# Kernel optimization log

Hardware: AMD Instinct MI355X
Metric: run time of the kernel (lower is better)

## Reference

```python
import jax, jax.numpy as jnp
import numpy as np
import math

KV_STRIDE = 2
Q_STRIDE = 1
WAVE_LEN = 1000.0
POS_MAG = 1.0


def _pos_embed(h, w, h_kv, w_kv, q_stride, kv_stride, feat_dim):
    # Sinusoidal relative-position embeddings, matching get_position_embedding.
    h_idx = jnp.arange(h, dtype=jnp.float32) * q_stride
    w_idx = jnp.arange(w, dtype=jnp.float32) * q_stride
    h_kv_idx = jnp.arange(h_kv, dtype=jnp.float32) * kv_stride
    w_kv_idx = jnp.arange(w_kv, dtype=jnp.float32) * kv_stride
    h_diff = (h_idx[:, None] - h_kv_idx[None, :]) * POS_MAG  # (h, h_kv)
    w_diff = (w_idx[:, None] - w_kv_idx[None, :]) * POS_MAG  # (w, w_kv)
    feat_range = jnp.arange(feat_dim // 4, dtype=jnp.float32)
    dim_mat = WAVE_LEN ** (4.0 / feat_dim * feat_range)  # (feat_dim//4,)
    wd = w_diff[:, :, None] / dim_mat  # (w, w_kv, F)
    hd = h_diff[:, :, None] / dim_mat  # (h, h_kv, F)
    emb_x = jnp.concatenate([jnp.sin(wd), jnp.cos(wd)], axis=2)  # (w, w_kv, feat_dim//2)
    emb_y = jnp.concatenate([jnp.sin(hd), jnp.cos(hd)], axis=2)  # (h, h_kv, feat_dim//2)
    return emb_x, emb_y


def setup_inputs() -> dict:
    key = jax.random.key(0)
    ks = jax.random.split(key, 11)
    C = 288
    s = 1.0 / math.sqrt(C)
    return {
        'x_input': jax.random.normal(ks[0], (2, C, 64, 64), jnp.float32),
        'Wq': jax.random.normal(ks[1], (C, C), jnp.float32) * s,
        'Wk': jax.random.normal(ks[2], (C, C), jnp.float32) * s,
        'Wv': jax.random.normal(ks[3], (C, C), jnp.float32) * s,
        'Wx': jax.random.normal(ks[4], (C, C // 2), jnp.float32) * s,
        'Wy': jax.random.normal(ks[5], (C, C // 2), jnp.float32) * s,
        'Wproj': jax.random.normal(ks[6], (C, C), jnp.float32) * s,
        'bproj': jax.random.normal(ks[7], (C,), jnp.float32) * 0.02,
        'Wc': jax.random.normal(ks[8], (9, C), jnp.float32) * s,
        'bc': jax.random.normal(ks[9], (9,), jnp.float32) * 0.02,
        'gamma': jax.random.normal(ks[10], (1,), jnp.float32),
    }


def reference(x_input, Wq, Wk, Wv, Wx, Wy, Wproj, bproj, Wc, bc, gamma):
    M = Wc.shape[0]                       # num_mixtures
    n, C, h, w = x_input.shape
    d = Wq.shape[0] // M                  # qk_embed_dim (== v_dim)
    x_q = x_input                         # q_stride == 1
    x_kv = x_input[:, :, ::KV_STRIDE, ::KV_STRIDE]  # AvgPool2d(k=1, stride=2)
    h_kv, w_kv = x_kv.shape[2], x_kv.shape[3]

    # 1x1 convs as channel GEMMs
    q = jnp.einsum('nchw,oc->nohw', x_q, Wq).reshape(n, M, d, h * w)
    q = q.transpose(0, 1, 3, 2)                                    # (n,M,hw,d)
    k = jnp.einsum('nchw,oc->nohw', x_kv, Wk).reshape(n, M, d, h_kv * w_kv)

    emb_x, emb_y = _pos_embed(h, w, h_kv, w_kv, Q_STRIDE, KV_STRIDE, C)
    inv_sqrt2 = 1.0 / math.sqrt(2.0)
    pf_x = (emb_x @ Wx.T).reshape(w, w_kv, M, d).transpose(2, 0, 1, 3) * inv_sqrt2  # (M,w,w_kv,d)
    pf_y = (emb_y @ Wy.T).reshape(h, h_kv, M, d).transpose(2, 0, 1, 3) * inv_sqrt2  # (M,h,h_kv,d)

    energy = jnp.matmul(q, k).reshape(n, M, h, w, h_kv, w_kv)
    q5 = q.reshape(n, M, h, w, d)
    e_x = jnp.einsum('nmhwd,mwvd->nmhwv', q5, pf_x)  # (n,M,h,w,w_kv)
    e_y = jnp.einsum('nmhwd,mhud->nmhwu', q5, pf_y)  # (n,M,h,w,h_kv)
    energy = energy + e_x[:, :, :, :, None, :] + e_y[:, :, :, :, :, None]
    energy = energy.reshape(n, M, h * w, h_kv * w_kv)
    attn = jax.nn.softmax(energy, axis=3)

    # Learned per-mixture gating from mean query context
    context = q.transpose(0, 1, 3, 2).reshape(n, M * d, h * w).mean(axis=2)  # (n, M*d)
    mix_w = jax.nn.softmax(context @ Wc.T + bc, axis=1)                      # (n, M)
    attn = jnp.sum(attn * mix_w[:, :, None, None], axis=1)                   # (n,hw,hw_kv)

    v = jnp.einsum('nchw,oc->nohw', x_kv, Wv).reshape(n, M * d, h_kv * w_kv)
    v = v.transpose(0, 2, 1)                                                 # (n,hw_kv,M*d)
    out = jnp.matmul(attn, v).transpose(0, 2, 1).reshape(n, M * d, h, w)
    out = jnp.einsum('nchw,oc->nohw', out, Wproj) + bproj[None, :, None, None]
    return gamma[0] * out + x_input
```

## Files before the change

kernel.cpp:

```cpp
#include <hip/hip_runtime.h>
#include <math.h>

#define NB     2
#define CDIM   288
#define HW     4096
#define PKV    1024
#define MHEAD  9
#define DHEAD  32

typedef __attribute__((ext_vector_type(8))) short bf16x8;
typedef __attribute__((ext_vector_type(4))) float f32x4;
typedef __attribute__((ext_vector_type(2))) unsigned int u32x2;
typedef __attribute__((ext_vector_type(4))) unsigned int u32x4;

#if __has_builtin(__builtin_amdgcn_exp2f)
#define EXP2(x) __builtin_amdgcn_exp2f(x)
#else
#define EXP2(x) exp2f(x)
#endif

__device__ inline unsigned short f2bf(float x) {
    unsigned int u = __float_as_uint(x);
    u = (u + 0x7fffu + ((u >> 16) & 1u)) >> 16;
    return (unsigned short)u;
}

__device__ inline void nt_store_u2(unsigned short* p, u32x2 v) {
    __builtin_nontemporal_store(v, (u32x2*)p);
}
__device__ inline void nt_store_u4(unsigned short* p, u32x4 v) {
    __builtin_nontemporal_store(v, (u32x4*)p);
}
__device__ inline void nt_store_bf8(unsigned short* p, bf16x8 v) {
    __builtin_nontemporal_store(v, (bf16x8*)p);
}


__global__ __launch_bounds__(256) void prep(const float* __restrict__ X,
        const float* __restrict__ Wq, const float* __restrict__ Wk,
        const float* __restrict__ Wv, const float* __restrict__ Wproj,
        unsigned short* __restrict__ XF, unsigned short* __restrict__ WFq,
        unsigned short* __restrict__ WFk, unsigned short* __restrict__ WFv,
        unsigned short* __restrict__ WFp, float* __restrict__ MX) {
    __shared__ float t32[32][133];
    __shared__ float red[4];
    int b = blockIdx.x;
    int tid = threadIdx.x;
    if (b < 576) {
        int bx = b % 32, by = (b / 32) % 9, n = b / 288;
        int j0 = bx * 128, c0 = by * 32;
        int c = tid >> 3, f = tid & 7;
        const float* src = &X[((size_t)n * CDIM + c0 + c) * HW + j0];
#pragma unroll
        for (int l = 0; l < 4; ++l) {
            float4 v = *(const float4*)&src[(f + l * 8) * 4];
            *(float4*)&t32[c][(f + l * 8) * 4] = v;
        }
        __syncthreads();
        int cc = c0 >> 5;
#pragma unroll
        for (int l = 0; l < 4; ++l) {
            int g = l * 256 + tid;
            int s = g >> 7;
            int w = g & 127;
            int lane = w >> 1, e0 = (w & 1) * 4;
            int jl = s * 16 + (lane & 15);
            int cb = (lane >> 4) * 8 + e0;
            unsigned int w0 = f2bf(t32[cb + 0][jl]) | ((unsigned int)f2bf(t32[cb + 1][jl]) << 16);
            unsigned int w1 = f2bf(t32[cb + 2][jl]) | ((unsigned int)f2bf(t32[cb + 3][jl]) << 16);
            int jt = (j0 >> 4) + s;
            unsigned short* O = XF + (size_t)n * HW * CDIM + ((size_t)jt * 9 + cc) * 512 + lane * 8 + e0;
            u32x2 pk = { w0, w1 };
            nt_store_u2(O, pk);
        }
    } else if (b < 738) {
        int t = b - 576;
        int sub = tid >> 6, lane = tid & 63;
        int ot = t / 9, cc = t % 9;
        const float* W = (sub == 0) ? Wq : (sub == 1) ? Wk : (sub == 2) ? Wv : Wproj;
        unsigned short* O = ((sub == 0) ? WFq : (sub == 1) ? WFk : (sub == 2) ? WFv : WFp)
                            + (size_t)t * 512;
        int o  = ot * 16 + (lane & 15);
        int c0 = cc * 32 + (lane >> 4) * 8;
        const float* src = W + (size_t)o * CDIM + c0;
        float4 f0 = *(const float4*)src, f1 = *(const float4*)(src + 4);
        unsigned int v0 = f2bf(f0.x) | ((unsigned int)f2bf(f0.y) << 16);
        unsigned int v1 = f2bf(f0.z) | ((unsigned int)f2bf(f0.w) << 16);
        unsigned int v2 = f2bf(f1.x) | ((unsigned int)f2bf(f1.y) << 16);
        unsigned int v3 = f2bf(f1.z) | ((unsigned int)f2bf(f1.w) << 16);
        u32x4 pk = { v0, v1, v2, v3 };
        nt_store_u4(O + lane * 8, pk);
    } else {
        int bid = b - 738;
        const float* xr = X + (size_t)bid * HW;
        float s = 0.f;
        for (int j = tid; j < HW; j += 256) s += xr[j];
        for (int off = 32; off > 0; off >>= 1) s += __shfl_xor(s, off, 64);
        if ((tid & 63) == 0) red[tid >> 6] = s;
        __syncthreads();
        if (tid == 0) MX[bid] = (red[0] + red[1] + red[2] + red[3]) * (1.f / 4096.f);
    }
}

__global__ __launch_bounds__(256) void mid(
        const float* __restrict__ Wx, const float* __restrict__ Wy,
        unsigned short* __restrict__ FXb, unsigned short* __restrict__ FYb,
        const float* __restrict__ Wq, const float* __restrict__ MX,
        const float* __restrict__ Wc, const float* __restrict__ bc,
        float* __restrict__ MIXW,
        const unsigned short* __restrict__ WFq, const unsigned short* __restrict__ WFk,
        const unsigned short* __restrict__ WFv, const unsigned short* __restrict__ XF,
        unsigned short* __restrict__ Qf, unsigned short* __restrict__ KF,
        unsigned short* __restrict__ VF) {
    __shared__ float emb[144];
    __shared__ float ctx_s[NB * CDIM];
    __shared__ float lg[18];
    __shared__ __attribute__((aligned(16))) unsigned short tr[4][32][40];
    int b = blockIdx.x;
    int tid = threadIdx.x;

    if (b < 252) {
        int axis = b / 126;
        int dif  = b % 126;
        float diff = (float)(dif - 62);
        if (tid < 72) {
            float dm = expf(6.9077552789821368f * ((float)tid * (1.f / 72.f)));
            float t  = diff / dm;
            emb[tid]      = sinf(t);
            emb[72 + tid] = cosf(t);
        }
        __syncthreads();
        const float* W = axis ? Wy : Wx;
        unsigned short* F = axis ? FYb : FXb;
        for (int o = tid; o < CDIM; o += 256) {
            const float* wr = W + (size_t)o * 144;
            float s = 0.f;
#pragma unroll 9
            for (int f4 = 0; f4 < 36; ++f4) {
                float4 w4 = *(const float4*)&wr[f4 * 4];
                s += emb[f4 * 4 + 0] * w4.x + emb[f4 * 4 + 1] * w4.y
                   + emb[f4 * 4 + 2] * w4.z + emb[f4 * 4 + 3] * w4.w;
            }
            int m = o >> 5, d = o & 31;
            F[(size_t)(m * 8 + (dif >> 4)) * 512 + ((dif & 15) + 16 * (d >> 3)) * 8 + (d & 7)]
                = f2bf(s * 0.70710678118654752f);
        }
    } else if (b == 252) {
        for (int idx = tid; idx < 1152; idx += 256) {
            int d = idx & 31, rr = (idx >> 5) & 1, mm = (idx >> 6) % 9, ax = idx / 576;
            int dif = 126 + rr;
            unsigned short* F = ax ? FYb : FXb;
            F[(size_t)(mm * 8 + 7) * 512 + ((dif & 15) + 16 * (d >> 3)) * 8 + (d & 7)] = 0;
        }
        for (int p = tid; p < NB * CDIM; p += 256) {
            int n = p / CDIM, o = p % CDIM;
            const float* wr = Wq + (size_t)o * CDIM;
            const float* mx = MX + n * CDIM;
            float s = 0.f;
            for (int c = 0; c < CDIM; c += 4) {
                float4 w4 = *(const float4*)&wr[c];
                float4 m4 = *(const float4*)&mx[c];
                s += w4.x * m4.x + w4.y * m4.y + w4.z * m4.z + w4.w * m4.w;
            }
            ctx_s[p] = s;
        }
        __syncthreads();
        if (tid < 18) {
            int n = tid / 9, j = tid % 9;
            float s = bc[j];
            for (int o = 0; o < CDIM; ++o) s += ctx_s[n * CDIM + o] * Wc[j * CDIM + o];
            lg[tid] = s;
        }
        __syncthreads();
        if (tid < 2) {
            float mx = -1e30f;
            for (int j = 0; j < 9; ++j) mx = fmaxf(mx, lg[tid * 9 + j]);
            float e[9], sm = 0.f;
            for (int j = 0; j < 9; ++j) { e[j] = __expf(lg[tid * 9 + j] - mx); sm += e[j]; }
            for (int j = 0; j < 9; ++j) MIXW[tid * 9 + j] = e[j] / sm;
        }
    } else {
        int bx = b - 253;
        int gx = bx % 40;
        int m  = (bx / 40) % 9;
        int n  = bx / 360;
        int wv = tid >> 6, lane = tid & 63;
        int lq = lane & 15, quad = lane >> 4;
        if (gx < 32) {
            int j0 = gx * 128;
            int jw = j0 + wv * 32;
            const unsigned short* Wb = WFq + ((size_t)(m * 2) * 9) * 512 + lane * 8;
            const unsigned short* Xb = XF + (size_t)n * HW * CDIM + ((size_t)(jw >> 4) * 9) * 512 + lane * 8;
            f32x4 acc[2][2] = {};
#pragma unroll
            for (int cc = 0; cc < 9; ++cc) {
                bf16x8 a0 = *(const bf16x8*)(Wb + (size_t)cc * 512);
                bf16x8 a1 = *(const bf16x8*)(Wb + (size_t)(9 + cc) * 512);
                bf16x8 b0 = *(const bf16x8*)(Xb + (size_t)cc * 512);
                bf16x8 b1 = *(const bf16x8*)(Xb + (size_t)(9 + cc) * 512);
                acc[0][0] = __builtin_amdgcn_mfma_f32_16x16x32_bf16(a0, b0, acc[0][0], 0, 0, 0);
                acc[0][1] = __builtin_amdgcn_mfma_f32_16x16x32_bf16(a0, b1, acc[0][1], 0, 0, 0);
                acc[1][0] = __builtin_amdgcn_mfma_f32_16x16x32_bf16(a1, b0, acc[1][0], 0, 0, 0);
                acc[1][1] = __builtin_amdgcn_mfma_f32_16x16x32_bf16(a1, b1, acc[1][1], 0, 0, 0);
            }
#pragma unroll
            for (int oi = 0; oi < 2; ++oi)
#pragma unroll
                for (int ji = 0; ji < 2; ++ji)
#pragma unroll
                    for (int r = 0; r < 4; ++r)
                        tr[wv][ji * 16 + lq][oi * 16 + quad * 4 + r]
                            = f2bf(1.4426950408889634f * acc[oi][ji][r]);
            int jl = lane & 31, half = lane >> 5;
            bf16x8 v0 = *(const bf16x8*)&tr[wv][jl][half * 16];
            bf16x8 v1 = *(const bf16x8*)&tr[wv][jl][half * 16 + 8];
            unsigned short* Qm = Qf + ((size_t)(n * MHEAD + m) * HW + jw + jl) * 32 + half * 16;
            nt_store_bf8(Qm, v0);
            nt_store_bf8(Qm + 8, v1);
        } else {
            int p0 = (gx - 32) * 128;
            int pw = p0 + wv * 32;
            const unsigned short* XFn = XF + (size_t)n * HW * CDIM;
            size_t bidx[2];
#pragma unroll
            for (int pi = 0; pi < 2; ++pi) {
                int p   = pw + pi * 16 + lq;
                int pos = ((p >> 5) << 7) + ((p & 31) << 1);
                bidx[pi] = ((size_t)(pos >> 4) * 9) * 512 + ((pos & 15) + 16 * quad) * 8;
            }
            const unsigned short* Wkb = WFk + ((size_t)(m * 2) * 9) * 512 + lane * 8;
            const unsigned short* Wvb = WFv + ((size_t)(m * 2) * 9) * 512 + lane * 8;
            f32x4 ak[2][2] = {}, av[2][2] = {};
#pragma unroll
            for (int cc = 0; cc < 9; ++cc) {
                bf16x8 a0k = *(const bf16x8*)(Wkb + (size_t)cc * 512);
                bf16x8 a1k = *(const bf16x8*)(Wkb + (size_t)(9 + cc) * 512);
                bf16x8 a0v = *(const bf16x8*)(Wvb + (size_t)cc * 512);
                bf16x8 a1v = *(const bf16x8*)(Wvb + (size_t)(9 + cc) * 512);
                bf16x8 b0  = *(const bf16x8*)(XFn + bidx[0] + (size_t)cc * 512);
                bf16x8 b1  = *(const bf16x8*)(XFn + bidx[1] + (size_t)cc * 512);
                ak[0][0] = __builtin_amdgcn_mfma_f32_16x16x32_bf16(a0k, b0, ak[0][0], 0, 0, 0);
                ak[0][1] = __builtin_amdgcn_mfma_f32_16x16x32_bf16(a0k, b1, ak[0][1], 0, 0, 0);
                ak[1][0] = __builtin_amdgcn_mfma_f32_16x16x32_bf16(a1k, b0, ak[1][0], 0, 0, 0);
                ak[1][1] = __builtin_amdgcn_mfma_f32_16x16x32_bf16(a1k, b1, ak[1][1], 0, 0, 0);
                av[0][0] = __builtin_amdgcn_mfma_f32_16x16x32_bf16(a0v, b0, av[0][0], 0, 0, 0);
                av[0][1] = __builtin_amdgcn_mfma_f32_16x16x32_bf16(a0v, b1, av[0][1], 0, 0, 0);
                av[1][0] = __builtin_amdgcn_mfma_f32_16x16x32_bf16(a1v, b0, av[1][0], 0, 0, 0);
                av[1][1] = __builtin_amdgcn_mfma_f32_16x16x32_bf16(a1v, b1, av[1][1], 0, 0, 0);
            }
#pragma unroll
            for (int oi = 0; oi < 2; ++oi)
#pragma unroll
                for (int pi = 0; pi < 2; ++pi)
#pragma unroll
                    for (int r = 0; r < 4; ++r)
                        tr[wv][pi * 16 + lq][oi * 16 + quad * 4 + r] = f2bf(ak[oi][pi][r]);
            unsigned short* KFm = KF + (size_t)(n * MHEAD + m) * (PKV * 32);
#pragma unroll
            for (int pi = 0; pi < 2; ++pi) {
                bf16x8 v = *(const bf16x8*)&tr[wv][pi * 16 + lq][quad * 8];
                nt_store_bf8(KFm + (size_t)((pw >> 4) + pi) * 512 + lane * 8, v);
            }
#pragma unroll
            for (int oi = 0; oi < 2; ++oi)
#pragma unroll
                for (int pi = 0; pi < 2; ++pi)
#pragma unroll
                    for (int r = 0; r < 4; ++r)
                        tr[wv][oi * 16 + quad * 4 + r][pi * 16 + lq] = f2bf(av[oi][pi][r]);
            unsigned short* VFn = VF + (size_t)n * CDIM * PKV;
#pragma unroll
            for (int oi = 0; oi < 2; ++oi) {
                bf16x8 v = *(const bf16x8*)&tr[wv][oi * 16 + lq][quad * 8];
                nt_store_bf8(VFn + (size_t)((m * 2 + oi) * 32 + (pw >> 5)) * 512 + lane * 8, v);
            }
        }
    }
}

__global__ __launch_bounds__(1024, 4) void attn_fused9(
        const unsigned short* __restrict__ Qf, const unsigned short* __restrict__ KF,
        const unsigned short* __restrict__ VF, const unsigned short* __restrict__ WFp,
        const unsigned short* __restrict__ FXb, const unsigned short* __restrict__ FYb,
        const float* __restrict__ MIXW, const float* __restrict__ bproj,
        const float* __restrict__ x, const float* __restrict__ gamma,
        float* __restrict__ OUT) {
    int n    = blockIdx.x >> 7;
    int i0   = (blockIdx.x & 127) * 32;
    int tid  = threadIdx.x;
    int wv   = tid >> 6;
    int ti   = wv >> 3;
    int w8   = wv & 7;
    int lane = tid & 63;
    int lq   = lane & 15;
    int quad = lane >> 4;
    int it0  = i0 + ti * 16;

    int bx_t = (it0 & 63) >> 4;
    int hh   = i0 >> 6;
    int by_t = hh >> 4;
    int dh   = hh & 15;

    __shared__ __attribute__((aligned(16))) unsigned short tr[32][1032];
    float (*Rx_s)[2][16][82] = reinterpret_cast<float (*)[2][16][82]>((char*)&tr[0][0]);
    float (*Ry_s)[2][16][82] = reinterpret_cast<float (*)[2][16][82]>((char*)&tr[0][0] + 20992);
    float (*ws_s)[2][16][8]  = reinterpret_cast<float (*)[2][16][8]>((char*)&tr[0][0] + 41984);
    unsigned short (*Mt)[296] = reinterpret_cast<unsigned short (*)[296]>(&tr[0][0]);

    float mixed[8][4];
#pragma unroll
    for (int t = 0; t < 8; ++t)
#pragma unroll
        for (int j = 0; j < 4; ++j) mixed[t][j] = 0.f;

    auto r_phase = [&](int mm, bf16x8 af) {
        int pp = mm & 1;
        if (w8 < 5) {
            bf16x8 bR = *(const bf16x8*)(FXb + (size_t)(mm * 8 + bx_t + w8) * 512 + lane * 8);
            f32x4 r = (f32x4){0.f, 0.f, 0.f, 0.f};
            r = __builtin_amdgcn_mfma_f32_16x16x32_bf16(af, bR, r, 0, 0, 0);
#pragma unroll
            for (int reg = 0; reg < 4; ++reg)
                Rx_s[pp][ti][quad * 4 + reg][w8 * 16 + lq] = r[reg];
        } else {
            bf16x8 bR = *(const bf16x8*)(FYb + (size_t)(mm * 8 + by_t + (w8 - 5)) * 512 + lane * 8);
            f32x4 r = (f32x4){0.f, 0.f, 0.f, 0.f};
            r = __builtin_amdgcn_mfma_f32_16x16x32_bf16(af, bR, r, 0, 0, 0);
#pragma unroll
            for (int reg = 0; reg < 4; ++reg)
                Ry_s[pp][ti][quad * 4 + reg][(w8 - 5) * 16 + lq] = r[reg];
        }
        if (w8 < 2) {
            bf16x8 bR = *(const bf16x8*)(FYb + (size_t)(mm * 8 + by_t + 3 + w8) * 512 + lane * 8);
            f32x4 r = (f32x4){0.f, 0.f, 0.f, 0.f};
            r = __builtin_amdgcn_mfma_f32_16x16x32_bf16(af, bR, r, 0, 0, 0);
#pragma unroll
            for (int reg = 0; reg < 4; ++reg)
                Ry_s[pp][ti][quad * 4 + reg][(3 + w8) * 16 + lq] = r[reg];
        }
    };

    bf16x8 af_cur = *(const bf16x8*)(Qf + (((size_t)n * MHEAD) * HW + it0 + lq) * 32 + quad * 8);
    r_phase(0, af_cur);
    __syncthreads();

#pragma unroll 1
    for (int m = 0; m < MHEAD; ++m) {
        const unsigned short* KmF = KF + (size_t)(n * MHEAD + m) * (PKV * 32);
        bf16x8 kf[8];
#pragma unroll
        for (int t = 0; t < 8; ++t)
            kf[t] = *(const bf16x8*)(KmF + (size_t)(w8 * 8 + t) * 512 + lane * 8);

        bf16x8 af_nxt = af_cur;
        __builtin_amdgcn_s_setprio(1);
        if (m + 1 < MHEAD) {
            af_nxt = *(const bf16x8*)(Qf + (((size_t)(n * MHEAD + m + 1)) * HW + it0 + lq) * 32 + quad * 8);
            r_phase(m + 1, af_nxt);
        }
        f32x4 acc[8];
#pragma unroll
        for (int t = 0; t < 8; ++t) {
            f32x4 z = (f32x4){0.f, 0.f, 0.f, 0.f};
            acc[t] = __builtin_amdgcn_mfma_f32_16x16x32_bf16(af_cur, kf[t], z, 0, 0, 0);
        }
        __builtin_amdgcn_s_setprio(0);

        int par = m & 1;
        float exA[4], exB[4];
#pragma unroll
        for (int j = 0; j < 4; ++j) {
            int q = quad * 4 + j;
            exA[j] = Rx_s[par][ti][q][q + 62 - 2 * lq];
            exB[j] = Rx_s[par][ti][q][q + 30 - 2 * lq];
        }
        float rs[4] = {0.f, 0.f, 0.f, 0.f};
#pragma unroll
        for (int tp = 0; tp < 4; ++tp) {
            int u = w8 * 4 + tp;
            float ey[4];
#pragma unroll
            for (int j = 0; j < 4; ++j) ey[j] = Ry_s[par][ti][quad * 4 + j][dh + 62 - 2 * u];
#pragma unroll
            for (int half = 0; half < 2; ++half) {
                int t = tp * 2 + half;
#pragma unroll
                for (int j = 0; j < 4; ++j) {
                    float e = EXP2(acc[t][j] + (half ? exB[j] : exA[j]) + ey[j]);
                    rs[j] += e;
                    acc[t][j] = e;
                }
            }
        }
#pragma unroll
        for (int j = 0; j < 4; ++j) {
            rs[j] += __shfl_xor(rs[j], 1, 64);
            rs[j] += __shfl_xor(rs[j], 2, 64);
            rs[j] += __shfl_xor(rs[j], 4, 64);
            rs[j] += __shfl_xor(rs[j], 8, 64);
        }
        if (lq == 0) {
#pragma unroll
            for (int j = 0; j < 4; ++j) ws_s[par][ti][quad * 4 + j][w8] = rs[j];
        }
        __syncthreads();

        {
            float wm = MIXW[n * MHEAD + m];
#pragma unroll
            for (int j = 0; j < 4; ++j) {
                int q = quad * 4 + j;
                float4 w0 = *(const float4*)&ws_s[par][ti][q][0];
                float4 w1 = *(const float4*)&ws_s[par][ti][q][4];
                float lt = (w0.x + w0.y) + (w0.z + w0.w) + (w1.x + w1.y) + (w1.z + w1.w);
                float fct = wm / lt;
#pragma unroll
                for (int t = 0; t < 8; ++t) mixed[t][j] += acc[t][j] * fct;
            }
        }
        __builtin_amdgcn_sched_barrier(0);
        af_cur = af_nxt;
    }

    __syncthreads();

#pragma unroll
    for (int t = 0; t < 8; ++t)
#pragma unroll
        for (int j = 0; j < 4; ++j)
            tr[ti * 16 + quad * 4 + j][w8 * 128 + t * 16 + lq] = f2bf(mixed[t][j]);
    __syncthreads();

    const unsigned short* VFn = VF + (size_t)n * CDIM * PKV;
    f32x4 accpv[2][2];
#pragma unroll
    for (int oi = 0; oi < 2; ++oi)
#pragma unroll
        for (int t2 = 0; t2 < 2; ++t2) accpv[oi][t2] = (f32x4){0.f, 0.f, 0.f, 0.f};
    bool has2 = (wv < 2);
#pragma unroll 4
    for (int pc = 0; pc < 32; ++pc) {
        bf16x8 pf0 = *(const bf16x8*)&tr[lq][pc * 32 + quad * 8];
        bf16x8 pf1 = *(const bf16x8*)&tr[16 + lq][pc * 32 + quad * 8];
        bf16x8 vf0 = *(const bf16x8*)(VFn + (size_t)(wv * 32 + pc) * 512 + lane * 8);
        accpv[0][0] = __builtin_amdgcn_mfma_f32_16x16x32_bf16(pf0, vf0, accpv[0][0], 0, 0, 0);
        accpv[0][1] = __builtin_amdgcn_mfma_f32_16x16x32_bf16(pf1, vf0, accpv[0][1], 0, 0, 0);
        if (has2) {
            bf16x8 vf1 = *(const bf16x8*)(VFn + (size_t)((wv + 16) * 32 + pc) * 512 + lane * 8);
            accpv[1][0] = __builtin_amdgcn_mfma_f32_16x16x32_bf16(pf0, vf1, accpv[1][0], 0, 0, 0);
            accpv[1][1] = __builtin_amdgcn_mfma_f32_16x16x32_bf16(pf1, vf1, accpv[1][1], 0, 0, 0);
        }
    }
    __syncthreads();

#pragma unroll
    for (int oi = 0; oi < 2; ++oi) {
        if (oi == 1 && !has2) continue;
        int ot = wv + oi * 16;
#pragma unroll
        for (int t2 = 0; t2 < 2; ++t2)
#pragma unroll
            for (int r = 0; r < 4; ++r)
                Mt[t2 * 16 + quad * 4 + r][ot * 16 + lq] = f2bf(accpv[oi][t2][r]);
    }
    __syncthreads();

    float g = gamma[0];
#pragma unroll
    for (int idx = 0; idx < 3; ++idx) {
        int ot = w8 + idx * 8;
        if (ot >= 18) continue;
        f32x4 acco = (f32x4){0.f, 0.f, 0.f, 0.f};
#pragma unroll
        for (int cc = 0; cc < 9; ++cc) {
            bf16x8 af = *(const bf16x8*)(WFp + (size_t)(ot * 9 + cc) * 512 + lane * 8);
            bf16x8 bfm = *(const bf16x8*)&Mt[ti * 16 + lq][cc * 32 + quad * 8];
            acco = __builtin_amdgcn_mfma_f32_16x16x32_bf16(af, bfm, acco, 0, 0, 0);
        }
#pragma unroll
        for (int r = 0; r < 4; ++r) {
            int o = ot * 16 + quad * 4 + r;
            size_t id = ((size_t)(n * CDIM) + o) * HW + it0 + lq;
            OUT[id] = g * (acco[r] + bproj[o]) + x[id];
        }
    }
}

extern "C" void kernel_launch(void* const* d_in, const int* in_sizes, int n_in,
                              void* d_out, int out_size, void* d_ws, size_t ws_size,
                              hipStream_t stream) {
    const float* x     = (const float*)d_in[0];
    const float* Wq    = (const float*)d_in[1];
    const float* Wk    = (const float*)d_in[2];
    const float* Wv    = (const float*)d_in[3];
    const float* Wx    = (const float*)d_in[4];
    const float* Wy    = (const float*)d_in[5];
    const float* Wproj = (const float*)d_in[6];
    const float* bproj = (const float*)d_in[7];
    const float* Wc    = (const float*)d_in[8];
    const float* bc    = (const float*)d_in[9];
    const float* gamma = (const float*)d_in[10];
    float* out = (float*)d_out;

    float* ws = (float*)d_ws;
    size_t off = 0;
    unsigned short* Qf  = (unsigned short*)(ws + off); off += (size_t)NB * MHEAD * HW * 32 / 2;
    unsigned short* KF  = (unsigned short*)(ws + off); off += (size_t)NB * MHEAD * PKV * 32 / 2;
    unsigned short* VF  = (unsigned short*)(ws + off); off += (size_t)NB * CDIM * PKV / 2;
    unsigned short* WFq = (unsigned short*)(ws + off); off += (size_t)CDIM * CDIM / 2;
    unsigned short* WFk = (unsigned short*)(ws + off); off += (size_t)CDIM * CDIM / 2;
    unsigned short* WFv = (unsigned short*)(ws + off); off += (size_t)CDIM * CDIM / 2;
    unsigned short* WFp = (unsigned short*)(ws + off); off += (size_t)CDIM * CDIM / 2;
    unsigned short* XF  = (unsigned short*)(ws + off); off += (size_t)NB * HW * CDIM / 2;
    unsigned short* FXb = (unsigned short*)(ws + off); off += (size_t)MHEAD * 8 * 512 / 2;
    unsigned short* FYb = (unsigned short*)(ws + off); off += (size_t)MHEAD * 8 * 512 / 2;
    float* MX   = ws + off; off += NB * CDIM;
    float* MIXW = ws + off; off += 32;

    prep<<<1314, 256, 0, stream>>>(x, Wq, Wk, Wv, Wproj,
                                   XF, WFq, WFk, WFv, WFp, MX);
    mid<<<973, 256, 0, stream>>>(Wx, Wy, FXb, FYb, Wq, MX, Wc, bc, MIXW,
                                 WFq, WFk, WFv, XF, Qf, KF, VF);
    attn_fused9<<<NB * HW / 32, 1024, 0, stream>>>(Qf, KF, VF, WFp, FXb, FYb, MIXW,
                                                   bproj, x, gamma, out);
}
```

Measured before the change: 186.1 us.

## Fuse channel-mean into transpose pass and move pos-embed projection to prep

The per-channel mean of x is now computed as partial sums during the bf16 transpose pass in prep, so the separate blocks that re-read all of x are gone. The mid kernel finishes the reduction from the partial sums. The sinusoidal position-embedding projection blocks move from mid into prep, which shortens mid's critical path. Non-temporal stores are replaced with ordinary stores so the bf16 intermediates can stay in cache for the next kernel.

```diff
diff --git a/kernel.cpp b/kernel.cpp
--- a/kernel.cpp
+++ b/kernel.cpp
@@ -10,8 +10,6 @@
 
 typedef __attribute__((ext_vector_type(8))) short bf16x8;
 typedef __attribute__((ext_vector_type(4))) float f32x4;
-typedef __attribute__((ext_vector_type(2))) unsigned int u32x2;
-typedef __attribute__((ext_vector_type(4))) unsigned int u32x4;
 
 #if __has_builtin(__builtin_amdgcn_exp2f)
 #define EXP2(x) __builtin_amdgcn_exp2f(x)
@@ -25,25 +23,17 @@
     return (unsigned short)u;
 }
 
-__device__ inline void nt_store_u2(unsigned short* p, u32x2 v) {
-    __builtin_nontemporal_store(v, (u32x2*)p);
-}
-__device__ inline void nt_store_u4(unsigned short* p, u32x4 v) {
-    __builtin_nontemporal_store(v, (u32x4*)p);
-}
-__device__ inline void nt_store_bf8(unsigned short* p, bf16x8 v) {
-    __builtin_nontemporal_store(v, (bf16x8*)p);
-}
-
 
 __global__ __launch_bounds__(256) void prep(const float* __restrict__ X,
         const float* __restrict__ Wq, const float* __restrict__ Wk,
         const float* __restrict__ Wv, const float* __restrict__ Wproj,
+        const float* __restrict__ Wx, const float* __restrict__ Wy,
         unsigned short* __restrict__ XF, unsigned short* __restrict__ WFq,
         unsigned short* __restrict__ WFk, unsigned short* __restrict__ WFv,
-        unsigned short* __restrict__ WFp, float* __restrict__ MX) {
+        unsigned short* __restrict__ WFp, unsigned short* __restrict__ FXb,
+        unsigned short* __restrict__ FYb, float* __restrict__ MXP) {
     __shared__ float t32[32][133];
-    __shared__ float red[4];
+    __shared__ float emb[144];
     int b = blockIdx.x;
     int tid = threadIdx.x;
     if (b < 576) {
@@ -51,11 +41,17 @@
         int j0 = bx * 128, c0 = by * 32;
         int c = tid >> 3, f = tid & 7;
         const float* src = &X[((size_t)n * CDIM + c0 + c) * HW + j0];
+        float psum = 0.f;
 #pragma unroll
         for (int l = 0; l < 4; ++l) {
             float4 v = *(const float4*)&src[(f + l * 8) * 4];
             *(float4*)&t32[c][(f + l * 8) * 4] = v;
-        }
+            psum += (v.x + v.y) + (v.z + v.w);
+        }
+        psum += __shfl_xor(psum, 1, 64);
+        psum += __shfl_xor(psum, 2, 64);
+        psum += __shfl_xor(psum, 4, 64);
+        if (f == 0) MXP[((size_t)n * CDIM + c0 + c) * 32 + bx] = psum;
         __syncthreads();
         int cc = c0 >> 5;
 #pragma unroll
@@ -70,8 +66,8 @@
             unsigned int w1 = f2bf(t32[cb + 2][jl]) | ((unsigned int)f2bf(t32[cb + 3][jl]) << 16);
             int jt = (j0 >> 4) + s;
             unsigned short* O = XF + (size_t)n * HW * CDIM + ((size_t)jt * 9 + cc) * 512 + lane * 8 + e0;
-            u32x2 pk = { w0, w1 };
-            nt_store_u2(O, pk);
+            uint2 pk = { w0, w1 };
+            *(uint2*)O = pk;
         }
     } else if (b < 738) {
         int t = b - 576;
@@ -88,40 +84,12 @@
         unsigned int v1 = f2bf(f0.z) | ((unsigned int)f2bf(f0.w) << 16);
         unsigned int v2 = f2bf(f1.x) | ((unsigned int)f2bf(f1.y) << 16);
         unsigned int v3 = f2bf(f1.z) | ((unsigned int)f2bf(f1.w) << 16);
-        u32x4 pk = { v0, v1, v2, v3 };
-        nt_store_u4(O + lane * 8, pk);
-    } else {
-        int bid = b - 738;
-        const float* xr = X + (size_t)bid * HW;
-        float s = 0.f;
-        for (int j = tid; j < HW; j += 256) s += xr[j];
-        for (int off = 32; off > 0; off >>= 1) s += __shfl_xor(s, off, 64);
-        if ((tid & 63) == 0) red[tid >> 6] = s;
-        __syncthreads();
-        if (tid == 0) MX[bid] = (red[0] + red[1] + red[2] + red[3]) * (1.f / 4096.f);
-    }
-}
-
-__global__ __launch_bounds__(256) void mid(
-        const float* __restrict__ Wx, const float* __restrict__ Wy,
-        unsigned short* __restrict__ FXb, unsigned short* __restrict__ FYb,
-        const float* __restrict__ Wq, const float* __restrict__ MX,
-        const float* __restrict__ Wc, const float* __restrict__ bc,
-        float* __restrict__ MIXW,
-        const unsigned short* __restrict__ WFq, const unsigned short* __restrict__ WFk,
-        const unsigned short* __restrict__ WFv, const unsigned short* __restrict__ XF,
-        unsigned short* __restrict__ Qf, unsigned short* __restrict__ KF,
-        unsigned short* __restrict__ VF) {
-    __shared__ float emb[144];
-    __shared__ float ctx_s[NB * CDIM];
-    __shared__ float lg[18];
-    __shared__ __attribute__((aligned(16))) unsigned short tr[4][32][40];
-    int b = blockIdx.x;
-    int tid = threadIdx.x;
-
-    if (b < 252) {
-        int axis = b / 126;
-        int dif  = b % 126;
+        uint4 pk = { v0, v1, v2, v3 };
+        *(uint4*)(O + lane * 8) = pk;
+    } else if (b < 990) {
+        int u = b - 738;
+        int axis = u / 126;
+        int dif  = u % 126;
         float diff = (float)(dif - 62);
         if (tid < 72) {
             float dm = expf(6.9077552789821368f * ((float)tid * (1.f / 72.f)));
@@ -145,17 +113,47 @@
             F[(size_t)(m * 8 + (dif >> 4)) * 512 + ((dif & 15) + 16 * (d >> 3)) * 8 + (d & 7)]
                 = f2bf(s * 0.70710678118654752f);
         }
-    } else if (b == 252) {
+    } else {
         for (int idx = tid; idx < 1152; idx += 256) {
             int d = idx & 31, rr = (idx >> 5) & 1, mm = (idx >> 6) % 9, ax = idx / 576;
             int dif = 126 + rr;
             unsigned short* F = ax ? FYb : FXb;
             F[(size_t)(mm * 8 + 7) * 512 + ((dif & 15) + 16 * (d >> 3)) * 8 + (d & 7)] = 0;
         }
+    }
+}
+
+__global__ __launch_bounds__(256) void mid(
+        const float* __restrict__ Wq, const float* __restrict__ MXP,
+        const float* __restrict__ Wc, const float* __restrict__ bc,
+        float* __restrict__ MIXW,
+        const unsigned short* __restrict__ WFq, const unsigned short* __restrict__ WFk,
+        const unsigned short* __restrict__ WFv, const unsigned short* __restrict__ XF,
+        unsigned short* __restrict__ Qf, unsigned short* __restrict__ KF,
+        unsigned short* __restrict__ VF) {
+    __shared__ float mxs[NB * CDIM];
+    __shared__ float ctx_s[NB * CDIM];
+    __shared__ float lg[18];
+    __shared__ __attribute__((aligned(16))) unsigned short tr[4][32][40];
+    int b = blockIdx.x;
+    int tid = threadIdx.x;
+
+    if (b == 0) {
+        for (int idx = tid; idx < NB * CDIM; idx += 256) {
+            const float* pp = &MXP[(size_t)idx * 32];
+            float s = 0.f;
+#pragma unroll
+            for (int k = 0; k < 32; k += 4) {
+                float4 v = *(const float4*)&pp[k];
+                s += (v.x + v.y) + (v.z + v.w);
+            }
+            mxs[idx] = s * (1.f / 4096.f);
+        }
+        __syncthreads();
         for (int p = tid; p < NB * CDIM; p += 256) {
             int n = p / CDIM, o = p % CDIM;
             const float* wr = Wq + (size_t)o * CDIM;
-            const float* mx = MX + n * CDIM;
+            const float* mx = &mxs[n * CDIM];
             float s = 0.f;
             for (int c = 0; c < CDIM; c += 4) {
                 float4 w4 = *(const float4*)&wr[c];
@@ -180,7 +178,7 @@
             for (int j = 0; j < 9; ++j) MIXW[tid * 9 + j] = e[j] / sm;
         }
     } else {
-        int bx = b - 253;
+        int bx = b - 1;
         int gx = bx % 40;
         int m  = (bx / 40) % 9;
         int n  = bx / 360;
@@ -215,8 +213,8 @@
             bf16x8 v0 = *(const bf16x8*)&tr[wv][jl][half * 16];
             bf16x8 v1 = *(const bf16x8*)&tr[wv][jl][half * 16 + 8];
             unsigned short* Qm = Qf + ((size_t)(n * MHEAD + m) * HW + jw + jl) * 32 + half * 16;
-            nt_store_bf8(Qm, v0);
-            nt_store_bf8(Qm + 8, v1);
+            *(bf16x8*)Qm = v0;
+            *(bf16x8*)(Qm + 8) = v1;
         } else {
             int p0 = (gx - 32) * 128;
             int pw = p0 + wv * 32;
@@ -259,7 +257,7 @@
 #pragma unroll
             for (int pi = 0; pi < 2; ++pi) {
                 bf16x8 v = *(const bf16x8*)&tr[wv][pi * 16 + lq][quad * 8];
-                nt_store_bf8(KFm + (size_t)((pw >> 4) + pi) * 512 + lane * 8, v);
+                *(bf16x8*)(KFm + (size_t)((pw >> 4) + pi) * 512 + lane * 8) = v;
             }
 #pragma unroll
             for (int oi = 0; oi < 2; ++oi)
@@ -272,13 +270,13 @@
 #pragma unroll
             for (int oi = 0; oi < 2; ++oi) {
                 bf16x8 v = *(const bf16x8*)&tr[wv][oi * 16 + lq][quad * 8];
-                nt_store_bf8(VFn + (size_t)((m * 2 + oi) * 32 + (pw >> 5)) * 512 + lane * 8, v);
+                *(bf16x8*)(VFn + (size_t)((m * 2 + oi) * 32 + (pw >> 5)) * 512 + lane * 8) = v;
             }
         }
     }
 }
 
-__global__ __launch_bounds__(1024, 4) void attn_fused9(
+__global__ __launch_bounds__(1024, 4) void attn_fused10(
         const unsigned short* __restrict__ Qf, const unsigned short* __restrict__ KF,
         const unsigned short* __restrict__ VF, const unsigned short* __restrict__ WFp,
         const unsigned short* __restrict__ FXb, const unsigned short* __restrict__ FYb,
@@ -514,13 +512,13 @@
     unsigned short* XF  = (unsigned short*)(ws + off); off += (size_t)NB * HW * CDIM / 2;
     unsigned short* FXb = (unsigned short*)(ws + off); off += (size_t)MHEAD * 8 * 512 / 2;
     unsigned short* FYb = (unsigned short*)(ws + off); off += (size_t)MHEAD * 8 * 512 / 2;
-    float* MX   = ws + off; off += NB * CDIM;
+    float* MXP  = ws + off; off += (size_t)NB * CDIM * 32;
     float* MIXW = ws + off; off += 32;
 
-    prep<<<1314, 256, 0, stream>>>(x, Wq, Wk, Wv, Wproj,
-                                   XF, WFq, WFk, WFv, WFp, MX);
-    mid<<<973, 256, 0, stream>>>(Wx, Wy, FXb, FYb, Wq, MX, Wc, bc, MIXW,
+    prep<<<991, 256, 0, stream>>>(x, Wq, Wk, Wv, Wproj, Wx, Wy,
+                                  XF, WFq, WFk, WFv, WFp, FXb, FYb, MXP);
+    mid<<<721, 256, 0, stream>>>(Wq, MXP, Wc, bc, MIXW,
                                  WFq, WFk, WFv, XF, Qf, KF, VF);
-    attn_fused9<<<NB * HW / 32, 1024, 0, stream>>>(Qf, KF, VF, WFp, FXb, FYb, MIXW,
-                                                   bproj, x, gamma, out);
+    attn_fused10<<<NB * HW / 32, 1024, 0, stream>>>(Qf, KF, VF, WFp, FXb, FYb, MIXW,
+                                                    bproj, x, gamma, out);
 }
```

After: 173.0 us. 1.08x faster.
